# Optimization experiments

Hardware: AMD Instinct MI355X
Metric: run time of the kernel (lower is better)

Reference implementation:

```python
import jax, jax.numpy as jnp
import numpy as np
from jax import lax

K = 8            # number of object slots
H = 250          # hidden / fc_size
EPS = 1e-5
DN = ('NCHW', 'OIHW', 'NCHW')


def ln_all(x):
    # F.layer_norm over all non-batch dims, no affine params (torch init: w=1,b=0)
    ax = tuple(range(1, x.ndim))
    m = jnp.mean(x, ax, keepdims=True)
    v = jnp.var(x, ax, keepdims=True)
    return (x - m) * lax.rsqrt(v + EPS)


def ln_last(x):
    # nn.LayerNorm(feat) -> last dim only
    m = jnp.mean(x, -1, keepdims=True)
    v = jnp.var(x, -1, keepdims=True)
    return (x - m) * lax.rsqrt(v + EPS)


def conv(x, w, b):
    # torch Conv2d(k=4, s=2, p=1), NCHW
    y = lax.conv_general_dilated(x, w, (2, 2), [(1, 1), (1, 1)], dimension_numbers=DN)
    return y + b[None, :, None, None]


def up4(x):
    return jnp.repeat(jnp.repeat(x, 4, axis=2), 4, axis=3)


def setup_inputs():
    ks = jax.random.split(jax.random.key(0), 20)
    bk = 48 * K
    p = lambda i, shape, s: jax.random.normal(ks[i], shape, jnp.float32) * s
    z = lambda n: jnp.zeros((n,), jnp.float32)
    return dict(
        x=p(0, (bk, 4096), 1.0),
        state=p(1, (bk, H), 1.0),
        # encoder convs (OIHW) + fc
        c1w=p(2, (16, 1, 4, 4), 0.25), c1b=z(16),
        c2w=p(3, (32, 16, 4, 4), 0.06), c2b=z(32),
        c3w=p(4, (64, 32, 4, 4), 0.04), c3b=z(64),
        efc_w=p(5, (4096, 512), 0.016), efc_b=z(512),
        # R_NEM (weights stored as [in, out])
        renc_w=p(6, (H, H), 0.06), renc_b=z(H),
        core_w=p(7, (2 * H, H), 0.045), core_b=z(H),
        ctx_w=p(8, (H, H), 0.06), ctx_b=z(H),
        att1_w=p(9, (H, 100), 0.06), att1_b=z(100),
        att2_w=p(10, (100, 1), 0.1), att2_b=z(1),
        out_w=p(11, (2 * H + 512, H), 0.03), out_b=z(H),
        # decoder fcs + convs
        dfc1_w=p(12, (H, 512), 0.06), dfc1_b=z(512),
        dfc2_w=p(13, (512, 4096), 0.045), dfc2_b=z(4096),
        d1w=p(14, (32, 64, 4, 4), 0.03), d1b=z(32),
        d2w=p(15, (16, 32, 4, 4), 0.045), d2b=z(16),
        d3w=p(16, (1, 16, 4, 4), 0.06), d3b=z(1),
    )


def reference(x, state, c1w, c1b, c2w, c2b, c3w, c3b, efc_w, efc_b,
              renc_w, renc_b, core_w, core_b, ctx_w, ctx_b,
              att1_w, att1_b, att2_w, att2_b, out_w, out_b,
              dfc1_w, dfc1_b, dfc2_w, dfc2_b, d1w, d1b, d2w, d2b, d3w, d3b):
    bk = x.shape[0]
    b = bk // K

    # ---------------- EncoderLayer ----------------
    def inwrap(h, w, bias):  # InputWrapper conv branch: NHWC -> permute(0,3,2,1) -> conv -> back
        y = conv(jnp.transpose(h, (0, 3, 2, 1)), w, bias)
        return jax.nn.elu(ln_all(jnp.transpose(y, (0, 3, 2, 1))))

    h = x.reshape(bk, 64, 64, 1)
    h = inwrap(h, c1w, c1b)                 # (bk,32,32,16)
    h = inwrap(h, c2w, c2b)                 # (bk,16,16,32)
    h = inwrap(h, c3w, c3b)                 # (bk,8,8,64)
    h = h.reshape(bk, -1)                   # (bk,4096)
    h = jax.nn.elu(ln_last(h @ efc_w + efc_b))   # (bk,512)

    # ---------------- R_NEM (RecurrentLayer) ----------------
    s1 = jax.nn.relu(ln_last(state @ renc_w + renc_b))   # (bk,H)
    s1r = s1.reshape(b, K, H)
    idx = np.array([[j for j in range(K) if j != i] for i in range(K)])  # (K,K-1)
    cs = s1r[:, idx, :]                                    # context: (b,K,K-1,H)
    fs = jnp.broadcast_to(s1r[:, :, None, :], cs.shape)    # focus copies
    pair = jnp.concatenate([fs, cs], axis=-1)              # (b,K,K-1,2H)
    core = jax.nn.relu(ln_last(pair @ core_w + core_b))    # (b,K,K-1,H)
    ctx = jax.nn.relu(ln_last(core @ ctx_w + ctx_b))       # (b,K,K-1,H)
    att = jax.nn.sigmoid(jnp.tanh(ln_last(core @ att1_w + att1_b)) @ att2_w + att2_b)  # (b,K,K-1,1)
    effect = jnp.sum(ctx * att, axis=2).reshape(bk, H)     # attention-weighted sum over K-1
    total = jnp.concatenate([s1, effect, h], axis=1)       # (bk, 2H+512)
    new_state = total @ out_w + out_b                      # (bk,H)
    xr = jax.nn.sigmoid(ln_last(new_state))
    state_out = jax.nn.sigmoid(new_state)

    # ---------------- DecoderLayer ----------------
    d = jax.nn.relu(ln_last(xr @ dfc1_w + dfc1_b))         # (bk,512)
    d = jax.nn.relu(ln_last(d @ dfc2_w + dfc2_b))          # (bk,4096)
    d = d.reshape(bk, 8, 8, 64)

    def outwrap(t, w, bias):
        y = conv(up4(jnp.transpose(t, (0, 3, 2, 1))), w, bias)
        return jnp.transpose(y, (0, 3, 2, 1))

    d = jax.nn.relu(ln_all(outwrap(d, d1w, d1b)))          # (bk,16,16,32)
    d = jax.nn.relu(ln_all(outwrap(d, d2w, d2b)))          # (bk,32,32,16)
    d = jax.nn.sigmoid(outwrap(d, d3w, d3b))               # (bk,64,64,1), no LN
    x_out = d.reshape(bk, -1)                              # (bk,4096)
    return x_out, state_out
```

## Files before the change

### kernel.cpp

```cpp
#include <hip/hip_runtime.h>
#include <hip/hip_bf16.h>
#include <math.h>

#define ST_ENC2 0
#define ST_ENC3 1
#define ST_DEC1 2
#define ST_DEC2 3
#define ST_ENC1 4

typedef __attribute__((ext_vector_type(8))) short bf16x8;
typedef __attribute__((ext_vector_type(4))) float f32x4;

__device__ __forceinline__ float eluf(float v){ return v > 0.f ? v : expm1f(v); }
__device__ __forceinline__ float sigf(float v){ return 1.f/(1.f+expf(-v)); }
__device__ __forceinline__ unsigned short f2bf(float f){
  unsigned u = __float_as_uint(f);
  u += 0x7FFFu + ((u >> 16) & 1u);
  return (unsigned short)(u >> 16);
}
__device__ __forceinline__ float bf2f(short s){
  return __uint_as_float(((unsigned)(unsigned short)s) << 16);
}

__device__ __forceinline__ void block_reduce2(float& a, float& b, float* sbuf){
  __syncthreads();
  for (int off = 32; off; off >>= 1){
    a += __shfl_down(a, off);
    b += __shfl_down(b, off);
  }
  int lane = threadIdx.x & 63, w = threadIdx.x >> 6;
  if (lane == 0){ sbuf[2*w] = a; sbuf[2*w+1] = b; }
  __syncthreads();
  if (threadIdx.x == 0){
    int nw = blockDim.x >> 6;
    float sa = 0.f, sb = 0.f;
    for (int i = 0; i < nw; i++){ sa += sbuf[2*i]; sb += sbuf[2*i+1]; }
    sbuf[0] = sa; sbuf[1] = sb;
  }
  __syncthreads();
  a = sbuf[0]; b = sbuf[1];
}
// ... 14 lines not shown
}
__device__ __forceinline__ void fold_elem(const float* __restrict__ w, float* __restrict__ CW,
                                          int O, int I, int l){
  int o = l % O; int q = l / O;
  int da = q & 1, db = (q>>1)&1, pa = (q>>2)&1, pb = (q>>3)&1, i = q>>4;
  CW[(((pb*2+pa)*4 + db*2+da)*I + i)*O + o] = fold_sum(w, O, I, o, i, pa, pb, da, db);
}
__device__ __forceinline__ void cvtc2_elem(const float* __restrict__ w, short* __restrict__ D, int l){
  int i = l & 15, t = (l>>4) & 15, o = l>>8;
  D[l] = (short)f2bf(w[(o*16 + i)*16 + t]);
}
__device__ __forceinline__ void cvtc3_elem(const float* __restrict__ w, short* __restrict__ D, int l){
  int i = l & 31, t = (l>>5) & 15, o = l>>9;
  D[l] = (short)f2bf(w[(o*32 + i)*16 + t]);
}
__device__ __forceinline__ void foldd1_elem(const float* __restrict__ w, short* __restrict__ D, int l){
  int i = l & 63, tap = (l>>6)&3, o = (l>>8)&31, ph = l>>13;
  D[l] = (short)f2bf(fold_sum(w, 32, 64, o, i, ph&1, ph>>1, tap&1, tap>>1));
}
__device__ __forceinline__ void foldd2_elem(const float* __restrict__ w, short* __restrict__ D, int l){
  int i = l & 31, tap = (l>>5)&3, o = (l>>7)&15, ph = l>>11;
  D[l] = (short)f2bf(fold_sum(w, 16, 32, o, i, ph&1, ph>>1, tap&1, tap>>1));
}

__global__ __launch_bounds__(256) void prep_combined(
  const float* __restrict__ efc,  short* __restrict__ Defc,
  const float* __restrict__ dfc2, short* __restrict__ Ddfc2,
  const float* __restrict__ outw, short* __restrict__ Dout,
  const float* __restrict__ corew,short* __restrict__ Dcore,
  const float* __restrict__ dfc1, short* __restrict__ Ddfc1,
  const float* __restrict__ renc, short* __restrict__ Drenc,
  const float* __restrict__ ctx,  short* __restrict__ Dctx,
  const float* __restrict__ att1, short* __restrict__ Datt1,
  float* __restrict__ stat,
  const float* __restrict__ d3w, float* __restrict__ CWT3,
  const float* __restrict__ c2w, short* __restrict__ BtC2,
  const float* __restrict__ c3w, short* __restrict__ BtC3,
  const float* __restrict__ d1w, short* __restrict__ BD1,
  const float* __restrict__ d2w, short* __restrict__ BD2,
  const float* __restrict__ state, short* __restrict__ SBF,
  short* __restrict__ TOTb)
{
  int bx = blockIdx.x;
  if (bx >= 1192){
    const int S0=3840, F3=S0+256, P2=F3+8192, P3=P2+32768, P4=P3+32768, P5=P4+8192,
              ST=P5+98304, TOTAL=ST+4608;
    for (int l = (bx-1192)*256 + threadIdx.x; l < TOTAL; l += 256*256){
      if (l < S0)      stat[l] = 0.f;
      else if (l < F3) fold_elem(d3w, CWT3, 1, 16, l - S0);
      else if (l < P2) cvtc2_elem(c2w, BtC2, l - F3);
      else if (l < P3) cvtc3_elem(c3w, BtC3, l - P2);
      else if (l < P4) foldd1_elem(d1w, BD1, l - P3);
      else if (l < P5) foldd2_elem(d2w, BD2, l - P4);
      else if (l < ST){
        int q = l - P5;
        int n = q >> 8, k = q & 255;
        SBF[q] = (k < 250) ? (short)f2bf(state[n*250 + k]) : (short)0;
      } else {
        int q = l - ST;
        int row = q / 12, cc = q % 12;
        int col = cc < 6 ? 250 + cc : 506 + (cc - 6);
        TOTb[row*1024 + col] = 0;
      }
    }
    return;
  }
  const float* W; short* D; int K, N, Kp, base, mode = 0;
  if      (bx < 512) { W=efc;  D=Defc;  K=4096; N=512;  Kp=4096; base=0;    }
  else if (bx < 1024){ W=dfc2; D=Ddfc2; K=512;  N=4096; Kp=512;  base=512;  }
  else if (bx < 1088){ W=outw; D=Dout;  K=1012; N=250;  Kp=1024; base=1024; mode=2; }
  else if (bx < 1120){ W=corew;D=Dcore; K=500;  N=250;  Kp=512;  base=1088; mode=1; }
  else if (bx < 1152){ W=dfc1; D=Ddfc1; K=250;  N=512;  Kp=256;  base=1120; }
  else if (bx < 1168){ W=renc; D=Drenc; K=250;  N=250;  Kp=256;  base=1152; }
  else if (bx < 1184){ W=ctx;  D=Dctx;  K=250;  N=250;  Kp=256;  base=1168; }
  else               { W=att1; D=Datt1; K=250;  N=100;  Kp=256;  base=1184; }
  int t = bx - base;
  int tpr = Kp >> 6;
  int tk = t % tpr, tn = t / tpr;
  __shared__ short tile[64][65];
  int c = threadIdx.x & 63, r4 = threadIdx.x >> 6;
  int n0 = tn*64, k0 = tk*64;
  #pragma unroll 4
  for (int p = 0; p < 16; p++){
    int r = r4*16 + p;
    int k = k0 + r, n = n0 + c;
    int ksrc = k; bool valid;
    if (mode == 0) valid = (k < K);
    else if (mode == 1){ valid = (k < 250) || (k >= 256 && k < 506); ksrc = k < 256 ? k : k - 6; }
    else { valid = (k < 250) || (k >= 256 && k < 506) || (k >= 512);
           ksrc = k < 256 ? k : (k < 512 ? k - 6 : k - 12); }
    float v = (valid && n < N) ? W[(size_t)ksrc*N + n] : 0.f;
    tile[c][r] = (short)f2bf(v);
  }
  __syncthreads();
  #pragma unroll 4
  for (int p = 0; p < 16; p++){
    int nn = r4*16 + p;
    int n = n0 + nn;
    if (n < N) D[(size_t)n*Kp + k0 + c] = tile[nn][c];
  }
}

__global__ __launch_bounds__(256) void cvt_ln_elu(
    const short* __restrict__ inb, const float* __restrict__ stat, short* __restrict__ outb)
{
  int n = blockIdx.x, tid = threadIdx.x;
  float sm = stat[n*2], sq = stat[n*2+1];
  float m = sm*(1.f/4096.f), rs = rsqrtf(sq*(1.f/4096.f) - m*m + 1e-5f);
  const short* ip = inb + (size_t)n*4096;
  short* op = outb + (size_t)n*4096;
  for (int l = tid*4; l < 4096; l += 1024){
    uint2 rv = *(const uint2*)&ip[l];
    float v0 = bf2f((short)(rv.x & 0xFFFF)), v1 = bf2f((short)(rv.x >> 16));
    float v2 = bf2f((short)(rv.y & 0xFFFF)), v3 = bf2f((short)(rv.y >> 16));
    uint2 pk;
    pk.x = f2bf(eluf((v0-m)*rs)) | ((unsigned)f2bf(eluf((v1-m)*rs))<<16);
    pk.y = f2bf(eluf((v2-m)*rs)) | ((unsigned)f2bf(eluf((v3-m)*rs))<<16);
    *(uint2*)&op[l] = pk;
  }
}

__global__ __launch_bounds__(256) void gemm_mfma(
    const short* __restrict__ Ab, const short* __restrict__ Bt,
    float* __restrict__ P, int M, int N, int Kp, int Kc)
{
  __shared__ __align__(16) short As[64*32];
  __shared__ __align__(16) short Bs[64*32];
  int tid = threadIdx.x;
  int bm = blockIdx.y*64, bn = blockIdx.x*64;
  int kb = blockIdx.z * Kc;
  int kend = kb + Kc;

  int r = tid >> 2, c = tid & 3;
  const short* Arow = Ab + (size_t)(bm + r)*Kp;
  int gn = bn + r;
  bool bval = gn < N;
  const short* Brow = Bt + (size_t)gn*Kp;

  uint4 hA, hB;
  auto load_regs = [&](int k0){
    hA = *(const uint4*)&Arow[k0 + c*8];
    hB = bval ? *(const uint4*)&Brow[k0 + c*8] : make_uint4(0,0,0,0);
  };
  auto write_lds = [&](){
    *(uint4*)&As[r*32 + c*8] = hA;
    *(uint4*)&Bs[r*32 + c*8] = hB;
  };

  int wave = tid >> 6;
  int ln = tid & 15, quad = (tid >> 4) & 3;
  int wr = (wave >> 1) * 32, wc = (wave & 1) * 32;

  f32x4 zero = {0.f, 0.f, 0.f, 0.f};
  f32x4 acc[2][2] = {{zero, zero}, {zero, zero}};
// ... 122 lines not shown
    float v = (rowbuf[c]-m)*r;
    if (act == 1) v = fmaxf(v, 0.f);
    else if (act == 2) v = eluf(v);
    else if (act == 3) v = tanhf(v);
    if (obf) ((short*)outp)[(size_t)row*os + c] = f2bf(v);
    else     ((float*)outp)[(size_t)row*os + c] = v;
  }
}

__global__ __launch_bounds__(256) void reduce_ns(
    const float* __restrict__ Pp, const float* __restrict__ bias,
    short* __restrict__ XRb, float* __restrict__ so, int M, int N, int KS)
{
  __shared__ float rowbuf[256];
  __shared__ float sbuf[16];
  int row = blockIdx.x;
  size_t MN = (size_t)M*N;
  float s = 0.f, s2 = 0.f;
  for (int c = threadIdx.x; c < N; c += 256){
    float v = bias[c];
    for (int ks = 0; ks < KS; ks++) v += Pp[ks*MN + (size_t)row*N + c];
    rowbuf[c] = v; s += v; s2 += v*v;
  }
  block_reduce2(s, s2, sbuf);
  float m = s / N;
  float r = rsqrtf(s2/N - m*m + 1e-5f);
  for (int c = threadIdx.x; c < N; c += 256){
    float v = rowbuf[c];
    XRb[(size_t)row*256 + c] = f2bf(sigf((v-m)*r));
    so[(size_t)row*N + c] = sigf(v);
  }
}

__global__ __launch_bounds__(256) void ctx_att_effect(
    const float* __restrict__ Pc, const float* __restrict__ ctx_b,
    const float* __restrict__ Pa, const float* __restrict__ att1_b,
    const float* __restrict__ w2, const float* __restrict__ b2,
    short* __restrict__ tot)
{
  __shared__ float ctxs[7][256];
  __shared__ float att_s[8];
  __shared__ float sbuf[16];
  int fi = blockIdx.x, tid = threadIdx.x;
  const size_t MN = (size_t)2688*250, MN2 = (size_t)2688*100;
  for (int jj = 0; jj < 7; jj++){
    int row = fi*7 + jj;
    float s = 0.f, s2 = 0.f, v = 0.f;
    if (tid < 250){
      v = ctx_b[tid] + Pc[(size_t)row*250 + tid] + Pc[MN + (size_t)row*250 + tid];
      s = v; s2 = v*v;
    }
    block_reduce2(s, s2, sbuf);
    float m = s*(1.f/250.f);
    float r = rsqrtf(s2*(1.f/250.f) - m*m + 1e-5f);
    if (tid < 250) ctxs[jj][tid] = fmaxf((v-m)*r, 0.f);
    float va = 0.f; s = 0.f; s2 = 0.f;
    if (tid < 100){
      va = att1_b[tid];
      #pragma unroll
      for (int ks = 0; ks < 4; ks++) va += Pa[ks*MN2 + (size_t)row*100 + tid];
      s = va; s2 = va*va;
    }
    block_reduce2(s, s2, sbuf);
    m = s*0.01f;
    r = rsqrtf(s2*0.01f - m*m + 1e-5f);
    float d = (tid < 100) ? tanhf((va-m)*r)*w2[tid] : 0.f;
    float dummy = 0.f;
    block_reduce2(d, dummy, sbuf);
    if (tid == 0) att_s[jj] = sigf(d + b2[0]);
  }
  __syncthreads();
  if (tid < 250){
    float s = 0.f;
    #pragma unroll
    for (int q = 0; q < 7; q++) s += ctxs[q][tid]*att_s[q];
    tot[(size_t)fi*1024 + 256 + tid] = f2bf(s);
  }
}

__global__ __launch_bounds__(256) void enc_conv1_ig(
    const float* __restrict__ x, const float* __restrict__ w, const float* __restrict__ bias,
    short* __restrict__ outp, float* __restrict__ stat)
{
  __shared__ __align__(16) float in_t[66*68];
  __shared__ float sbuf[16];
  int n = blockIdx.x, tid = threadIdx.x;
  for (int l = tid; l < 66*68; l += 256) in_t[l] = 0.f;
  __syncthreads();
  const float* xin = x + (size_t)n*4096;
  for (int l4 = tid; l4 < 1024; l4 += 256){
    float4 v = *(const float4*)&xin[l4*4];
    int aa = (l4*4) >> 6, bb = (l4*4) & 63;
    float* dst = &in_t[(aa+1)*68 + bb + 1];
    dst[0]=v.x; dst[1]=v.y; dst[2]=v.z; dst[3]=v.w;
  }
  int o = tid & 15;
  float wr[16];
  #pragma unroll
  for (int t = 0; t < 16; t++) wr[t] = w[o*16 + t];
  float bv = bias[o];
  __syncthreads();
  float s = 0.f, s2 = 0.f;
  short* op = outp + (size_t)n*16384;
  for (int r = 0; r < 64; r++){
    int idx = tid + (r<<8);
    int bq = (idx>>4)&31, aq = idx>>9;
    int a0 = 2*aq, b0 = 2*bq;
    float acc = bv;
    #pragma unroll
    for (int kw = 0; kw < 4; kw++){
      const float* row = &in_t[(a0+kw)*68 + b0];
      float2 p0 = *(const float2*)&row[0];
      float2 p1 = *(const float2*)&row[2];
      acc += p0.x*wr[0*4+kw] + p0.y*wr[1*4+kw] + p1.x*wr[2*4+kw] + p1.y*wr[3*4+kw];
    }
    op[idx] = f2bf(acc);
    s += acc; s2 += acc*acc;
  }
  block_reduce2(s, s2, sbuf);
  if (tid == 0){ atomicAdd(&stat[n*2], s); atomicAdd(&stat[n*2+1], s2); }
}

__global__ __launch_bounds__(256) void enc_conv2_mfma(
    const short* __restrict__ in, const short* __restrict__ Bt, const float* __restrict__ bias,
    const float* __restrict__ stat_in, short* __restrict__ outp, float* __restrict__ stat)
{
  __shared__ __align__(16) short in_t[34*34*16];
  __shared__ float sbuf[16];
  int n = blockIdx.x, tid = threadIdx.x;
  float smv = stat_in[n*2], sqv = stat_in[n*2+1];
  float m = smv*(1.f/16384.f), rs = rsqrtf(sqv*(1.f/16384.f) - m*m + 1e-5f);
  for (int l = tid; l < 34*34*16/4; l += 256) ((unsigned long long*)in_t)[l] = 0ull;
  __syncthreads();
  const short* ip = in + (size_t)n*16384;
  for (int l = tid; l < 4096; l += 256){
    int i4 = l & 3, bb = (l>>2) & 31, aa = l>>7;
    uint2 rv = *(const uint2*)&ip[aa*512 + bb*16 + i4*4];
    float v0 = bf2f((short)(rv.x & 0xFFFF)), v1 = bf2f((short)(rv.x >> 16));
    float v2 = bf2f((short)(rv.y & 0xFFFF)), v3 = bf2f((short)(rv.y >> 16));
    uint2 pk;
    pk.x = f2bf(eluf((v0-m)*rs)) | ((unsigned)f2bf(eluf((v1-m)*rs))<<16);
    pk.y = f2bf(eluf((v2-m)*rs)) | ((unsigned)f2bf(eluf((v3-m)*rs))<<16);
    *(uint2*)&in_t[((aa+1)*34 + (bb+1))*16 + i4*4] = pk;
  }
  int wave = tid>>6, ln = tid&15, quad = (tid>>4)&3;
  bf16x8 bfr[2][8];
  #pragma unroll
  for (int nt = 0; nt < 2; nt++){
    const short* Brow = Bt + (nt*16 + ln)*256;
    #pragma unroll
    for (int ks = 0; ks < 8; ks++)
      bfr[nt][ks] = *(const bf16x8*)&Brow[ks*32 + quad*8];
  }
  __syncthreads();
  f32x4 z = {0.f,0.f,0.f,0.f};
  f32x4 acc[2][4] = {{z,z,z,z},{z,z,z,z}};
  int tapq = quad>>1, io = (quad&1)*8;
  #pragma unroll
  for (int ks = 0; ks < 8; ks++){
    int t = 2*ks + tapq;
    int kh = t>>2, kw = t&3;
    #pragma unroll
    for (int mt = 0; mt < 4; mt++){
      int p = (wave*4 + mt)*16 + ln;
      int oa = p>>4, ob = p&15;
      bf16x8 a = *(const bf16x8*)&in_t[((2*oa+kw)*34 + (2*ob+kh))*16 + io];
      acc[0][mt] = __builtin_amdgcn_mfma_f32_16x16x32_bf16(a, bfr[0][ks], acc[0][mt],0,0,0);
      acc[1][mt] = __builtin_amdgcn_mfma_f32_16x16x32_bf16(a, bfr[1][ks], acc[1][mt],0,0,0);
    }
  }
  float s = 0.f, s2 = 0.f;
  short* op = outp + (size_t)n*8192;
  #pragma unroll
  for (int nt = 0; nt < 2; nt++){
    int o = nt*16 + ln;
    float bz = bias[o];
    #pragma unroll
    for (int mt = 0; mt < 4; mt++)
      #pragma unroll
      for (int j = 0; j < 4; j++){
        int p = (wave*4 + mt)*16 + quad*4 + j;
        float v = acc[nt][mt][j] + bz;
        s += v; s2 += v*v;
        int oa = p>>4, ob = p&15;
        op[oa*512 + ob*32 + o] = f2bf(v);
      }
  }
  block_reduce2(s, s2, sbuf);
  if (tid == 0){ atomicAdd(&stat[n*2], s); atomicAdd(&stat[n*2+1], s2); }
}

__global__ __launch_bounds__(256) void enc_conv3_mfma(
    const short* __restrict__ in, const short* __restrict__ Bt, const float* __restrict__ bias,
    const float* __restrict__ stat_in, short* __restrict__ outp, float* __restrict__ stat)
{
  __shared__ __align__(16) short in_t[18*18*32];
  __shared__ float sbuf[16];
  int n = blockIdx.x, tid = threadIdx.x;
  float smv = stat_in[n*2], sqv = stat_in[n*2+1];
  float m = smv*(1.f/8192.f), rs = rsqrtf(sqv*(1.f/8192.f) - m*m + 1e-5f);
  for (int l = tid; l < 18*18*32/4; l += 256) ((unsigned long long*)in_t)[l] = 0ull;
  __syncthreads();
  const short* ip = in + (size_t)n*8192;
  for (int l = tid; l < 2048; l += 256){
    int i4 = l & 7, bb = (l>>3)&15, aa = l>>7;
    uint2 rv = *(const uint2*)&ip[aa*512 + bb*32 + i4*4];
    float v0 = bf2f((short)(rv.x & 0xFFFF)), v1 = bf2f((short)(rv.x >> 16));
    float v2 = bf2f((short)(rv.y & 0xFFFF)), v3 = bf2f((short)(rv.y >> 16));
    uint2 pk;
    pk.x = f2bf(eluf((v0-m)*rs)) | ((unsigned)f2bf(eluf((v1-m)*rs))<<16);
    pk.y = f2bf(eluf((v2-m)*rs)) | ((unsigned)f2bf(eluf((v3-m)*rs))<<16);
    *(uint2*)&in_t[((aa+1)*18 + (bb+1))*32 + i4*4] = pk;
  }
  int wave = tid>>6, ln = tid&15, quad = (tid>>4)&3;
  int o = wave*16 + ln;
  bf16x8 bfr[16];
  {
    const short* Brow = Bt + o*512;
    #pragma unroll
    for (int ks = 0; ks < 16; ks++)
      bfr[ks] = *(const bf16x8*)&Brow[ks*32 + quad*8];
  }
  __syncthreads();
  f32x4 z = {0.f,0.f,0.f,0.f};
  f32x4 acc[4] = {z,z,z,z};
  #pragma unroll
  for (int ks = 0; ks < 16; ks++){
    int kh = ks>>2, kw = ks&3;
    #pragma unroll
    for (int mt = 0; mt < 4; mt++){
      int p = mt*16 + ln;
      int oa = p>>3, ob = p&7;
      bf16x8 a = *(const bf16x8*)&in_t[((2*oa+kw)*18 + (2*ob+kh))*32 + quad*8];
      acc[mt] = __builtin_amdgcn_mfma_f32_16x16x32_bf16(a, bfr[ks], acc[mt],0,0,0);
    }
  }
  float s = 0.f, s2 = 0.f;
  float bz = bias[o];
  short* op = outp + (size_t)n*4096;
  #pragma unroll
  for (int mt = 0; mt < 4; mt++)
    #pragma unroll
    for (int j = 0; j < 4; j++){
      int p = mt*16 + quad*4 + j;
      int oa = p>>3, ob = p&7;
      float v = acc[mt][j] + bz;
      s += v; s2 += v*v;
      op[oa*512 + ob*64 + o] = f2bf(v);
    }
  block_reduce2(s, s2, sbuf);
  if (tid == 0){ atomicAdd(&stat[n*2], s); atomicAdd(&stat[n*2+1], s2); }
}

__global__ __launch_bounds__(256) void dec_conv1_mfma(
    const short* __restrict__ in, const short* __restrict__ Bd, const float* __restrict__ bias,
    short* __restrict__ outp, float* __restrict__ stat)
{
  __shared__ __align__(16) short in_t[10*10*64];
  __shared__ float sbuf[16];
  int n = blockIdx.x, tid = threadIdx.x;
  for (int l = tid; l < 10*10*64/4; l += 256) ((unsigned long long*)in_t)[l] = 0ull;
  __syncthreads();
  const short* ip = in + (size_t)n*4096;
  for (int l = tid; l < 1024; l += 256){
    int i4 = l & 15, sb = (l>>4)&7, sa = l>>7;
    *(uint2*)&in_t[((sa+1)*10 + (sb+1))*64 + i4*4] = *(const uint2*)&ip[sa*512 + sb*64 + i4*4];
  }
  int wave = tid>>6, ln = tid&15, quad = (tid>>4)&3;
  int pa = wave & 1, pb = wave >> 1;
  bf16x8 bfr[2][8];
  #pragma unroll
  for (int nt = 0; nt < 2; nt++){
    const short* Brow = Bd + (wave*32 + nt*16 + ln)*256;
    #pragma unroll
    for (int ks = 0; ks < 8; ks++)
      bfr[nt][ks] = *(const bf16x8*)&Brow[ks*32 + quad*8];
  }
  __syncthreads();
  f32x4 z = {0.f,0.f,0.f,0.f};
  f32x4 acc[2][4] = {{z,z,z,z},{z,z,z,z}};
  #pragma unroll
  for (int ks = 0; ks < 8; ks++){
    int tap = ks>>1, ibase = (ks&1)*32 + quad*8;
    int da = tap & 1, db = tap >> 1;
    #pragma unroll
    for (int mt = 0; mt < 4; mt++){
      int p = mt*16 + ln;
      int ta = p>>3, tb = p&7;
      bf16x8 a = *(const bf16x8*)&in_t[((ta+da+pa)*10 + (tb+db+pb))*64 + ibase];
      acc[0][mt] = __builtin_amdgcn_mfma_f32_16x16x32_bf16(a, bfr[0][ks], acc[0][mt],0,0,0);
      acc[1][mt] = __builtin_amdgcn_mfma_f32_16x16x32_bf16(a, bfr[1][ks], acc[1][mt],0,0,0);
    }
  }
  float s = 0.f, s2 = 0.f;
  short* op = outp + (size_t)n*8192;
  #pragma unroll
  for (int nt = 0; nt < 2; nt++){
    int o = nt*16 + ln;
    float bz = bias[o];
    #pragma unroll
    for (int mt = 0; mt < 4; mt++)
      #pragma unroll
      for (int j = 0; j < 4; j++){
        int p = mt*16 + quad*4 + j;
        int ta = p>>3, tb = p&7;
        float v = acc[nt][mt][j] + bz;
        s += v; s2 += v*v;
        op[(2*ta+pa)*512 + (2*tb+pb)*32 + o] = f2bf(v);
      }
  }
  block_reduce2(s, s2, sbuf);
  if (tid == 0){ atomicAdd(&stat[n*2], s); atomicAdd(&stat[n*2+1], s2); }
}

__global__ __launch_bounds__(256) void dec_conv2_mfma(
    const short* __restrict__ in, const short* __restrict__ Bd, const float* __restrict__ bias,
    const float* __restrict__ stat_in, short* __restrict__ outp, float* __restrict__ stat)
{
  __shared__ __align__(16) short in_t[18*18*32];
  __shared__ float sbuf[16];
  int n = blockIdx.x, tid = threadIdx.x;
  float smv = stat_in[n*2], sqv = stat_in[n*2+1];
  float m = smv*(1.f/8192.f), rs = rsqrtf(sqv*(1.f/8192.f) - m*m + 1e-5f);
  for (int l = tid; l < 18*18*32/4; l += 256) ((unsigned long long*)in_t)[l] = 0ull;
  __syncthreads();
  const short* ip = in + (size_t)n*8192;
  for (int l = tid; l < 2048; l += 256){
    int i4 = l & 7, sb = (l>>3)&15, sa = l>>7;
    uint2 rv = *(const uint2*)&ip[sa*512 + sb*32 + i4*4];
    float v0 = bf2f((short)(rv.x & 0xFFFF)), v1 = bf2f((short)(rv.x >> 16));
    float v2 = bf2f((short)(rv.y & 0xFFFF)), v3 = bf2f((short)(rv.y >> 16));
    uint2 pk;
    pk.x = f2bf(fmaxf((v0-m)*rs,0.f)) | ((unsigned)f2bf(fmaxf((v1-m)*rs,0.f))<<16);
    pk.y = f2bf(fmaxf((v2-m)*rs,0.f)) | ((unsigned)f2bf(fmaxf((v3-m)*rs,0.f))<<16);
    *(uint2*)&in_t[((sa+1)*18 + (sb+1))*32 + i4*4] = pk;
  }
  int wave = tid>>6, ln = tid&15, quad = (tid>>4)&3;
  int pa = wave & 1, pb = wave >> 1;
  bf16x8 bfr[4];
  {
    const short* Brow = Bd + (wave*16 + ln)*128;
    #pragma unroll
    for (int ks = 0; ks < 4; ks++)
      bfr[ks] = *(const bf16x8*)&Brow[ks*32 + quad*8];
  }
  __syncthreads();
  f32x4 z = {0.f,0.f,0.f,0.f};
  f32x4 acc[16] = {z,z,z,z,z,z,z,z,z,z,z,z,z,z,z,z};
  #pragma unroll
  for (int ks = 0; ks < 4; ks++){
    int da = ks & 1, db = ks >> 1;
    #pragma unroll
    for (int mt = 0; mt < 16; mt++){
      int p = mt*16 + ln;
      int ta = p>>4, tb = p&15;
      bf16x8 a = *(const bf16x8*)&in_t[((ta+da+pa)*18 + (tb+db+pb))*32 + quad*8];
      acc[mt] = __builtin_amdgcn_mfma_f32_16x16x32_bf16(a, bfr[ks], acc[mt],0,0,0);
    }
  }
  float s = 0.f, s2 = 0.f;
  float bz = bias[ln];
  short* op = outp + (size_t)n*16384;
  #pragma unroll
  for (int mt = 0; mt < 16; mt++)
    #pragma unroll
    for (int j = 0; j < 4; j++){
      int p = mt*16 + quad*4 + j;
      int ta = p>>4, tb = p&15;
      float v = acc[mt][j] + bz;
      s += v; s2 += v*v;
      op[(2*ta+pa)*512 + (2*tb+pb)*16 + ln] = f2bf(v);
    }
  block_reduce2(s, s2, sbuf);
  if (tid == 0){ atomicAdd(&stat[n*2], s); atomicAdd(&stat[n*2+1], s2); }
}

__global__ __launch_bounds__(256) void dec_conv3_ig(
    const short* __restrict__ in, const float* __restrict__ CWT, const float* __restrict__ bias,
    const float* __restrict__ stat_in, float* __restrict__ outp)
{
  __shared__ __align__(16) float in_t[9792];
  __shared__ __align__(16) float wl[256];
  int bx = blockIdx.x;
  int n = bx >> 1, b0 = (bx & 1) * 32, tb0 = b0 >> 1;
  int tid = threadIdx.x;
  float sm = stat_in[n*2], sq = stat_in[n*2+1];
  float m = sm*(1.f/16384.f), rs = rsqrtf(sq*(1.f/16384.f) - m*m + 1e-5f);
  const short* ip = in + (size_t)n*16384;
  for (int l = tid; l < 9792; l += 256){
    int i = l & 15, sb = (l >> 4) % 18, sap = l / 288;
    int sa = sap - 1, sbg = tb0 - 1 + sb;
    float v = 0.f;
    if ((unsigned)sa < 32u && (unsigned)sbg < 32u)
      v = fmaxf((bf2f(ip[sa*512 + sbg*16 + i])-m)*rs, 0.f);
    in_t[(sap*18 + sb)*16 + i] = v;
  }
  for (int l = tid; l < 256; l += 256) wl[l] = CWT[l];
  __syncthreads();
  float bv = bias[0];
  int bl = tid & 31, ath = tid >> 5;
  int b = b0 + bl;
  int tb = b >> 1, pb = b & 1;
  float* op = outp + (size_t)n*4096;
  #pragma unroll
  for (int j = 0; j < 8; j++){
    int a = ath*8 + j;
    int ta = a >> 1, pa = a & 1;
    float4 s4 = make_float4(0.f,0.f,0.f,0.f);
    #pragma unroll
    for (int db = 0; db < 2; db++){
      int sb = tb + db + (pb ? 0 : -1);
      int sbl = sb - (tb0 - 1);
      #pragma unroll
      for (int da = 0; da < 2; da++){
        int sa = ta + da + (pa ? 0 : -1);
        int sap = sa + 1;
        const float4* A4 = (const float4*)&in_t[(sap*18 + sbl)*16];
        const float4* B4 = (const float4*)&wl[((pb*2+pa)*4 + db*2+da)*16];
        #pragma unroll
        for (int q = 0; q < 4; q++){
          float4 av = A4[q], bw = B4[q];
          s4.x += av.x*bw.x; s4.y += av.y*bw.y;
          s4.z += av.z*bw.z; s4.w += av.w*bw.w;
        }
      }
    }
    op[a*64 + b] = sigf(bv + s4.x + s4.y + s4.z + s4.w);
// ... 11 lines not shown
  const float* c2b    = (const float*)d_in[5];
  const float* c3w    = (const float*)d_in[6];
  const float* c3b    = (const float*)d_in[7];
  const float* efc_w  = (const float*)d_in[8];
  const float* efc_b  = (const float*)d_in[9];
  const float* renc_w = (const float*)d_in[10];
  const float* renc_b = (const float*)d_in[11];
  const float* core_w = (const float*)d_in[12];
  const float* core_b = (const float*)d_in[13];
  const float* ctx_w  = (const float*)d_in[14];
  const float* ctx_b  = (const float*)d_in[15];
  const float* att1_w = (const float*)d_in[16];
  const float* att1_b = (const float*)d_in[17];
  const float* att2_w = (const float*)d_in[18];
  const float* att2_b = (const float*)d_in[19];
  const float* out_w  = (const float*)d_in[20];
  const float* out_b  = (const float*)d_in[21];
  const float* dfc1_w = (const float*)d_in[22];
  const float* dfc1_b = (const float*)d_in[23];
  const float* dfc2_w = (const float*)d_in[24];
  const float* dfc2_b = (const float*)d_in[25];
  const float* d1w    = (const float*)d_in[26];
  const float* d1b    = (const float*)d_in[27];
  const float* d2w    = (const float*)d_in[28];
  const float* d2b    = (const float*)d_in[29];
  const float* d3w    = (const float*)d_in[30];
  const float* d3b    = (const float*)d_in[31];

  float* wsf = (float*)d_ws;
  size_t o = 0;
  float* PB   = wsf + o; o += (size_t)1600*1024;
  float* PB2  = wsf + o; o += (size_t)2688*100*4;
  float* CWT3 = wsf + o; o += 256;
  float* STAT = wsf + o; o += 5*384*2;
  short* E1b  = (short*)(wsf + o); o += (size_t)384*16384/2;
  short* E2b  = (short*)(wsf + o); o += (size_t)384*8192/2;
  short* E3b  = (short*)(wsf + o); o += (size_t)384*4096/2;
  short* TOTb = (short*)(wsf + o); o += (size_t)384*1024/2;
  short* C1b  = (short*)(wsf + o); o += (size_t)2688*256/2;
  short* XRb  = (short*)(wsf + o); o += (size_t)384*256/2;
  short* G1b  = (short*)(wsf + o); o += (size_t)384*512/2;
  short* ECV  = (short*)(wsf + o); o += (size_t)384*4096/2;
  short* SBF  = (short*)(wsf + o); o += (size_t)384*256/2;
  short* BtC2 = (short*)(wsf + o); o += 8192/2;
  short* BtC3 = (short*)(wsf + o); o += 32768/2;
  short* BD1  = (short*)(wsf + o); o += 32768/2;
  short* BD2  = (short*)(wsf + o); o += 8192/2;
  short* BT_efc  = (short*)(wsf + o); o += 2097152/2;
  short* BT_renc = (short*)(wsf + o); o += 64000/2;
  short* BT_core = (short*)(wsf + o); o += 128000/2;
  short* BT_ctx  = (short*)(wsf + o); o += 64000/2;
  short* BT_att1 = (short*)(wsf + o); o += 25600/2;
  short* BT_out  = (short*)(wsf + o); o += 256000/2;
  short* BT_dfc1 = (short*)(wsf + o); o += 131072/2;
  short* BT_dfc2 = (short*)(wsf + o); o += 2097152/2;
  short* D1b = E2b;
  short* D2b = E1b;
  short* G2b = E3b;

  float* xout = (float*)d_out;
  float* sout = xout + (size_t)384*4096;

  prep_combined<<<1448, 256, 0, stream>>>(
      efc_w, BT_efc, dfc2_w, BT_dfc2, out_w, BT_out, core_w, BT_core,
      dfc1_w, BT_dfc1, renc_w, BT_renc, ctx_w, BT_ctx, att1_w, BT_att1,
      STAT, d3w, CWT3, c2w, BtC2, c3w, BtC3, d1w, BD1, d2w, BD2, state, SBF, TOTb);

  enc_conv1_ig<<<384, 256, 0, stream>>>(x, c1w, c1b, E1b, STAT + ST_ENC1*768);
  enc_conv2_mfma<<<384, 256, 0, stream>>>(E1b, BtC2, c2b, STAT + ST_ENC1*768, E2b, STAT + ST_ENC2*768);
  enc_conv3_mfma<<<384, 256, 0, stream>>>(E2b, BtC3, c3b, STAT + ST_ENC2*768, E3b, STAT + ST_ENC3*768);
  cvt_ln_elu<<<384, 256, 0, stream>>>(E3b, STAT + ST_ENC3*768, ECV);
  gemm_mfma<<<dim3(8,6,8), 256, 0, stream>>>(ECV, BT_efc, PB, 384, 512, 4096, 512);
  reduce_ln<<<384, 256, 0, stream>>>(PB, efc_b, TOTb+512, 384, 512, 8, 1024, 2, 1);

  gemm_mfma<<<dim3(4,6,8), 256, 0, stream>>>(SBF, BT_renc, PB, 384, 250, 256, 32);
  reduce_ln<<<384, 256, 0, stream>>>(PB, renc_b, TOTb, 384, 250, 8, 1024, 1, 1);
  gemm_core_mfma<<<dim3(4,42,2), 256, 0, stream>>>(TOTb, BT_core, PB, 2688, 250, 256);
  reduce_ln<<<2688, 256, 0, stream>>>(PB, core_b, C1b, 2688, 250, 2, 256, 1, 1);
  gemm_mfma<<<dim3(4,42,2), 256, 0, stream>>>(C1b, BT_ctx, PB, 2688, 250, 256, 128);
  gemm_mfma<<<dim3(2,42,4), 256, 0, stream>>>(C1b, BT_att1, PB2, 2688, 100, 256, 64);
  ctx_att_effect<<<384, 256, 0, stream>>>(PB, ctx_b, PB2, att1_b, att2_w, att2_b, TOTb);

  gemm_mfma<<<dim3(4,6,8), 256, 0, stream>>>(TOTb, BT_out, PB, 384, 250, 1024, 128);
  reduce_ns<<<384, 256, 0, stream>>>(PB, out_b, XRb, sout, 384, 250, 8);

  gemm_mfma<<<dim3(8,6,4), 256, 0, stream>>>(XRb, BT_dfc1, PB, 384, 512, 256, 64);
  reduce_ln<<<384, 256, 0, stream>>>(PB, dfc1_b, G1b, 384, 512, 4, 512, 1, 1);
  gemm_mfma<<<dim3(64,6,1), 256, 0, stream>>>(G1b, BT_dfc2, PB, 384, 4096, 512, 512);
  reduce_ln<<<384, 256, 0, stream>>>(PB, dfc2_b, G2b, 384, 4096, 1, 4096, 1, 1);

  dec_conv1_mfma<<<384, 256, 0, stream>>>(G2b, BD1, d1b, D1b, STAT + ST_DEC1*768);
  dec_conv2_mfma<<<384, 256, 0, stream>>>(D1b, BD2, d2b, STAT + ST_DEC1*768, D2b, STAT + ST_DEC2*768);
  dec_conv3_ig<<<768, 256, 0, stream>>>(D2b, CWT3, d3b, STAT + ST_DEC2*768, xout);

  (void)in_sizes; (void)n_in; (void)out_size; (void)ws_size;
}
```

Baseline: 356.4 us.

## Apply per-sample LayerNorm in conv producers, drop stat atomics and cvt kernel

Each conv kernel already holds the whole per-sample output, so it now computes the LayerNorm statistics itself, normalizes, and writes the activated values. Consumers just copy them into LDS. This removes the global atomic stat buffer, its zeroing in the prep kernel, and the separate cvt_ln_elu launch. The attention kernel is also reworked to one wave per row with shuffle reductions instead of a serial loop of block reductions. In exchange, enc_conv1 gains a 32KB LDS staging buffer, which may lower occupancy.

```diff
diff --git a/kernel.cpp b/kernel.cpp
--- a/kernel.cpp
+++ b/kernel.cpp
@@ -1,12 +1,6 @@
 #include <hip/hip_runtime.h>
 #include <hip/hip_bf16.h>
 #include <math.h>
-
-#define ST_ENC2 0
-#define ST_ENC3 1
-#define ST_DEC1 2
-#define ST_DEC2 3
-#define ST_ENC1 4
 
 typedef __attribute__((ext_vector_type(8))) short bf16x8;
 typedef __attribute__((ext_vector_type(4))) float f32x4;
@@ -87,7 +81,6 @@
   const float* __restrict__ renc, short* __restrict__ Drenc,
   const float* __restrict__ ctx,  short* __restrict__ Dctx,
   const float* __restrict__ att1, short* __restrict__ Datt1,
-  float* __restrict__ stat,
   const float* __restrict__ d3w, float* __restrict__ CWT3,
   const float* __restrict__ c2w, short* __restrict__ BtC2,
   const float* __restrict__ c3w, short* __restrict__ BtC3,
@@ -98,11 +91,10 @@
 {
   int bx = blockIdx.x;
   if (bx >= 1192){
-    const int S0=3840, F3=S0+256, P2=F3+8192, P3=P2+32768, P4=P3+32768, P5=P4+8192,
+    const int F3=256, P2=F3+8192, P3=P2+32768, P4=P3+32768, P5=P4+8192,
               ST=P5+98304, TOTAL=ST+4608;
     for (int l = (bx-1192)*256 + threadIdx.x; l < TOTAL; l += 256*256){
-      if (l < S0)      stat[l] = 0.f;
-      else if (l < F3) fold_elem(d3w, CWT3, 1, 16, l - S0);
+      if (l < F3)      fold_elem(d3w, CWT3, 1, 16, l);
       else if (l < P2) cvtc2_elem(c2w, BtC2, l - F3);
       else if (l < P3) cvtc3_elem(c3w, BtC3, l - P2);
       else if (l < P4) foldd1_elem(d1w, BD1, l - P3);
@@ -156,25 +148,6 @@
   }
 }
 
-__global__ __launch_bounds__(256) void cvt_ln_elu(
-    const short* __restrict__ inb, const float* __restrict__ stat, short* __restrict__ outb)
-{
-  int n = blockIdx.x, tid = threadIdx.x;
-  float sm = stat[n*2], sq = stat[n*2+1];
-  float m = sm*(1.f/4096.f), rs = rsqrtf(sq*(1.f/4096.f) - m*m + 1e-5f);
-  const short* ip = inb + (size_t)n*4096;
-  short* op = outb + (size_t)n*4096;
-  for (int l = tid*4; l < 4096; l += 1024){
-    uint2 rv = *(const uint2*)&ip[l];
-    float v0 = bf2f((short)(rv.x & 0xFFFF)), v1 = bf2f((short)(rv.x >> 16));
-    float v2 = bf2f((short)(rv.y & 0xFFFF)), v3 = bf2f((short)(rv.y >> 16));
-    uint2 pk;
-    pk.x = f2bf(eluf((v0-m)*rs)) | ((unsigned)f2bf(eluf((v1-m)*rs))<<16);
-    pk.y = f2bf(eluf((v2-m)*rs)) | ((unsigned)f2bf(eluf((v3-m)*rs))<<16);
-    *(uint2*)&op[l] = pk;
-  }
-}
-
 __global__ __launch_bounds__(256) void gemm_mfma(
     const short* __restrict__ Ab, const short* __restrict__ Bt,
     float* __restrict__ P, int M, int N, int Kp, int Kc)
@@ -363,57 +336,79 @@
   }
 }
 
-__global__ __launch_bounds__(256) void ctx_att_effect(
+__global__ __launch_bounds__(448) void ctx_att_effect(
     const float* __restrict__ Pc, const float* __restrict__ ctx_b,
     const float* __restrict__ Pa, const float* __restrict__ att1_b,
     const float* __restrict__ w2, const float* __restrict__ b2,
     short* __restrict__ tot)
 {
-  __shared__ float ctxs[7][256];
-  __shared__ float att_s[8];
-  __shared__ float sbuf[16];
+  __shared__ float ctxs[7][250];
+  __shared__ float att_s[7];
   int fi = blockIdx.x, tid = threadIdx.x;
+  int jj = tid >> 6, lane = tid & 63;
   const size_t MN = (size_t)2688*250, MN2 = (size_t)2688*100;
-  for (int jj = 0; jj < 7; jj++){
-    int row = fi*7 + jj;
-    float s = 0.f, s2 = 0.f, v = 0.f;
-    if (tid < 250){
-      v = ctx_b[tid] + Pc[(size_t)row*250 + tid] + Pc[MN + (size_t)row*250 + tid];
-      s = v; s2 = v*v;
-    }
-    block_reduce2(s, s2, sbuf);
-    float m = s*(1.f/250.f);
-    float r = rsqrtf(s2*(1.f/250.f) - m*m + 1e-5f);
-    if (tid < 250) ctxs[jj][tid] = fmaxf((v-m)*r, 0.f);
-    float va = 0.f; s = 0.f; s2 = 0.f;
-    if (tid < 100){
-      va = att1_b[tid];
+  int row = fi*7 + jj;
+  float vv[4];
+  float s = 0.f, s2 = 0.f;
+  #pragma unroll
+  for (int t = 0; t < 4; t++){
+    int c = lane + t*64;
+    float v = 0.f;
+    if (c < 250) v = ctx_b[c] + Pc[(size_t)row*250 + c] + Pc[MN + (size_t)row*250 + c];
+    vv[t] = v; s += v; s2 += v*v;
+  }
+  #pragma unroll
+  for (int off = 32; off; off >>= 1){ s += __shfl_down(s, off); s2 += __shfl_down(s2, off); }
+  s = __shfl(s, 0); s2 = __shfl(s2, 0);
+  float m = s*(1.f/250.f);
+  float r = rsqrtf(s2*(1.f/250.f) - m*m + 1e-5f);
+  #pragma unroll
+  for (int t = 0; t < 4; t++){
+    int c = lane + t*64;
+    if (c < 250) ctxs[jj][c] = fmaxf((vv[t]-m)*r, 0.f);
+  }
+  float va[2];
+  s = 0.f; s2 = 0.f;
+  #pragma unroll
+  for (int t = 0; t < 2; t++){
+    int c = lane + t*64;
+    float v = 0.f;
+    if (c < 100){
+      v = att1_b[c];
       #pragma unroll
-      for (int ks = 0; ks < 4; ks++) va += Pa[ks*MN2 + (size_t)row*100 + tid];
-      s = va; s2 = va*va;
-    }
-    block_reduce2(s, s2, sbuf);
-    m = s*0.01f;
-    r = rsqrtf(s2*0.01f - m*m + 1e-5f);
-    float d = (tid < 100) ? tanhf((va-m)*r)*w2[tid] : 0.f;
-    float dummy = 0.f;
-    block_reduce2(d, dummy, sbuf);
-    if (tid == 0) att_s[jj] = sigf(d + b2[0]);
-  }
-  __syncthreads();
-  if (tid < 250){
-    float s = 0.f;
-    #pragma unroll
-    for (int q = 0; q < 7; q++) s += ctxs[q][tid]*att_s[q];
-    tot[(size_t)fi*1024 + 256 + tid] = f2bf(s);
+      for (int ks = 0; ks < 4; ks++) v += Pa[ks*MN2 + (size_t)row*100 + c];
+    }
+    va[t] = v; s += v; s2 += v*v;
+  }
+  #pragma unroll
+  for (int off = 32; off; off >>= 1){ s += __shfl_down(s, off); s2 += __shfl_down(s2, off); }
+  s = __shfl(s, 0); s2 = __shfl(s2, 0);
+  m = s*0.01f;
+  r = rsqrtf(s2*0.01f - m*m + 1e-5f);
+  float d = 0.f;
+  #pragma unroll
+  for (int t = 0; t < 2; t++){
+    int c = lane + t*64;
+    if (c < 100) d += tanhf((va[t]-m)*r)*w2[c];
+  }
+  #pragma unroll
+  for (int off = 32; off; off >>= 1) d += __shfl_down(d, off);
+  if (lane == 0) att_s[jj] = sigf(d + b2[0]);
+  __syncthreads();
+  for (int h = tid; h < 250; h += 448){
+    float sum = 0.f;
+    #pragma unroll
+    for (int q = 0; q < 7; q++) sum += ctxs[q][h]*att_s[q];
+    tot[(size_t)fi*1024 + 256 + h] = f2bf(sum);
   }
 }
 
 __global__ __launch_bounds__(256) void enc_conv1_ig(
     const float* __restrict__ x, const float* __restrict__ w, const float* __restrict__ bias,
-    short* __restrict__ outp, float* __restrict__ stat)
+    short* __restrict__ outp)
 {
   __shared__ __align__(16) float in_t[66*68];
+  __shared__ short rawb[16384];
   __shared__ float sbuf[16];
   int n = blockIdx.x, tid = threadIdx.x;
   for (int l = tid; l < 66*68; l += 256) in_t[l] = 0.f;
@@ -432,7 +427,6 @@
   float bv = bias[o];
   __syncthreads();
   float s = 0.f, s2 = 0.f;
-  short* op = outp + (size_t)n*16384;
   for (int r = 0; r < 64; r++){
     int idx = tid + (r<<8);
     int bq = (idx>>4)&31, aq = idx>>9;
@@ -445,34 +439,32 @@
       float2 p1 = *(const float2*)&row[2];
       acc += p0.x*wr[0*4+kw] + p0.y*wr[1*4+kw] + p1.x*wr[2*4+kw] + p1.y*wr[3*4+kw];
     }
-    op[idx] = f2bf(acc);
+    rawb[idx] = f2bf(acc);
     s += acc; s2 += acc*acc;
   }
   block_reduce2(s, s2, sbuf);
-  if (tid == 0){ atomicAdd(&stat[n*2], s); atomicAdd(&stat[n*2+1], s2); }
+  float m = s*(1.f/16384.f);
+  float rs = rsqrtf(s2*(1.f/16384.f) - m*m + 1e-5f);
+  short* op = outp + (size_t)n*16384;
+  for (int l = tid; l < 16384; l += 256){
+    float v = bf2f(rawb[l]);
+    op[l] = f2bf(eluf((v-m)*rs));
+  }
 }
 
 __global__ __launch_bounds__(256) void enc_conv2_mfma(
     const short* __restrict__ in, const short* __restrict__ Bt, const float* __restrict__ bias,
-    const float* __restrict__ stat_in, short* __restrict__ outp, float* __restrict__ stat)
+    short* __restrict__ outp)
 {
   __shared__ __align__(16) short in_t[34*34*16];
   __shared__ float sbuf[16];
   int n = blockIdx.x, tid = threadIdx.x;
-  float smv = stat_in[n*2], sqv = stat_in[n*2+1];
-  float m = smv*(1.f/16384.f), rs = rsqrtf(sqv*(1.f/16384.f) - m*m + 1e-5f);
   for (int l = tid; l < 34*34*16/4; l += 256) ((unsigned long long*)in_t)[l] = 0ull;
   __syncthreads();
   const short* ip = in + (size_t)n*16384;
   for (int l = tid; l < 4096; l += 256){
     int i4 = l & 3, bb = (l>>2) & 31, aa = l>>7;
-    uint2 rv = *(const uint2*)&ip[aa*512 + bb*16 + i4*4];
-    float v0 = bf2f((short)(rv.x & 0xFFFF)), v1 = bf2f((short)(rv.x >> 16));
-    float v2 = bf2f((short)(rv.y & 0xFFFF)), v3 = bf2f((short)(rv.y >> 16));
-    uint2 pk;
-    pk.x = f2bf(eluf((v0-m)*rs)) | ((unsigned)f2bf(eluf((v1-m)*rs))<<16);
-    pk.y = f2bf(eluf((v2-m)*rs)) | ((unsigned)f2bf(eluf((v3-m)*rs))<<16);
-    *(uint2*)&in_t[((aa+1)*34 + (bb+1))*16 + i4*4] = pk;
+    *(uint2*)&in_t[((aa+1)*34 + (bb+1))*16 + i4*4] = *(const uint2*)&ip[aa*512 + bb*16 + i4*4];
   }
   int wave = tid>>6, ln = tid&15, quad = (tid>>4)&3;
   bf16x8 bfr[2][8];
@@ -501,47 +493,48 @@
     }
   }
   float s = 0.f, s2 = 0.f;
+  #pragma unroll
+  for (int nt = 0; nt < 2; nt++){
+    float bz = bias[nt*16 + ln];
+    #pragma unroll
+    for (int mt = 0; mt < 4; mt++)
+      #pragma unroll
+      for (int j = 0; j < 4; j++){
+        float v = acc[nt][mt][j] + bz;
+        acc[nt][mt][j] = v; s += v; s2 += v*v;
+      }
+  }
+  block_reduce2(s, s2, sbuf);
+  float m = s*(1.f/8192.f);
+  float rs = rsqrtf(s2*(1.f/8192.f) - m*m + 1e-5f);
   short* op = outp + (size_t)n*8192;
   #pragma unroll
   for (int nt = 0; nt < 2; nt++){
     int o = nt*16 + ln;
-    float bz = bias[o];
     #pragma unroll
     for (int mt = 0; mt < 4; mt++)
       #pragma unroll
       for (int j = 0; j < 4; j++){
         int p = (wave*4 + mt)*16 + quad*4 + j;
-        float v = acc[nt][mt][j] + bz;
-        s += v; s2 += v*v;
         int oa = p>>4, ob = p&15;
-        op[oa*512 + ob*32 + o] = f2bf(v);
+        op[oa*512 + ob*32 + o] = f2bf(eluf((acc[nt][mt][j]-m)*rs));
       }
   }
-  block_reduce2(s, s2, sbuf);
-  if (tid == 0){ atomicAdd(&stat[n*2], s); atomicAdd(&stat[n*2+1], s2); }
 }
 
 __global__ __launch_bounds__(256) void enc_conv3_mfma(
     const short* __restrict__ in, const short* __restrict__ Bt, const float* __restrict__ bias,
-    const float* __restrict__ stat_in, short* __restrict__ outp, float* __restrict__ stat)
+    short* __restrict__ outp)
 {
   __shared__ __align__(16) short in_t[18*18*32];
   __shared__ float sbuf[16];
   int n = blockIdx.x, tid = threadIdx.x;
-  float smv = stat_in[n*2], sqv = stat_in[n*2+1];
-  float m = smv*(1.f/8192.f), rs = rsqrtf(sqv*(1.f/8192.f) - m*m + 1e-5f);
   for (int l = tid; l < 18*18*32/4; l += 256) ((unsigned long long*)in_t)[l] = 0ull;
   __syncthreads();
   const short* ip = in + (size_t)n*8192;
   for (int l = tid; l < 2048; l += 256){
     int i4 = l & 7, bb = (l>>3)&15, aa = l>>7;
-    uint2 rv = *(const uint2*)&ip[aa*512 + bb*32 + i4*4];
-    float v0 = bf2f((short)(rv.x & 0xFFFF)), v1 = bf2f((short)(rv.x >> 16));
-    float v2 = bf2f((short)(rv.y & 0xFFFF)), v3 = bf2f((short)(rv.y >> 16));
-    uint2 pk;
-    pk.x = f2bf(eluf((v0-m)*rs)) | ((unsigned)f2bf(eluf((v1-m)*rs))<<16);
-    pk.y = f2bf(eluf((v2-m)*rs)) | ((unsigned)f2bf(eluf((v3-m)*rs))<<16);
-    *(uint2*)&in_t[((aa+1)*18 + (bb+1))*32 + i4*4] = pk;
+    *(uint2*)&in_t[((aa+1)*18 + (bb+1))*32 + i4*4] = *(const uint2*)&ip[aa*512 + bb*32 + i4*4];
   }
   int wave = tid>>6, ln = tid&15, quad = (tid>>4)&3;
   int o = wave*16 + ln;
@@ -568,6 +561,16 @@
   }
   float s = 0.f, s2 = 0.f;
   float bz = bias[o];
+  #pragma unroll
+  for (int mt = 0; mt < 4; mt++)
+    #pragma unroll
+    for (int j = 0; j < 4; j++){
+      float v = acc[mt][j] + bz;
+      acc[mt][j] = v; s += v; s2 += v*v;
+    }
+  block_reduce2(s, s2, sbuf);
+  float m = s*(1.f/4096.f);
+  float rs = rsqrtf(s2*(1.f/4096.f) - m*m + 1e-5f);
   short* op = outp + (size_t)n*4096;
   #pragma unroll
   for (int mt = 0; mt < 4; mt++)
@@ -575,17 +578,13 @@
     for (int j = 0; j < 4; j++){
       int p = mt*16 + quad*4 + j;
       int oa = p>>3, ob = p&7;
-      float v = acc[mt][j] + bz;
-      s += v; s2 += v*v;
-      op[oa*512 + ob*64 + o] = f2bf(v);
-    }
-  block_reduce2(s, s2, sbuf);
-  if (tid == 0){ atomicAdd(&stat[n*2], s); atomicAdd(&stat[n*2+1], s2); }
+      op[oa*512 + ob*64 + o] = f2bf(eluf((acc[mt][j]-m)*rs));
+    }
 }
 
 __global__ __launch_bounds__(256) void dec_conv1_mfma(
     const short* __restrict__ in, const short* __restrict__ Bd, const float* __restrict__ bias,
-    short* __restrict__ outp, float* __restrict__ stat)
+    short* __restrict__ outp)
 {
   __shared__ __align__(16) short in_t[10*10*64];
   __shared__ float sbuf[16];
@@ -624,47 +623,48 @@
     }
   }
   float s = 0.f, s2 = 0.f;
+  #pragma unroll
+  for (int nt = 0; nt < 2; nt++){
+    float bz = bias[nt*16 + ln];
+    #pragma unroll
+    for (int mt = 0; mt < 4; mt++)
+      #pragma unroll
+      for (int j = 0; j < 4; j++){
+        float v = acc[nt][mt][j] + bz;
+        acc[nt][mt][j] = v; s += v; s2 += v*v;
+      }
+  }
+  block_reduce2(s, s2, sbuf);
+  float m = s*(1.f/8192.f);
+  float rs = rsqrtf(s2*(1.f/8192.f) - m*m + 1e-5f);
   short* op = outp + (size_t)n*8192;
   #pragma unroll
   for (int nt = 0; nt < 2; nt++){
     int o = nt*16 + ln;
-    float bz = bias[o];
     #pragma unroll
     for (int mt = 0; mt < 4; mt++)
       #pragma unroll
       for (int j = 0; j < 4; j++){
         int p = mt*16 + quad*4 + j;
         int ta = p>>3, tb = p&7;
-        float v = acc[nt][mt][j] + bz;
-        s += v; s2 += v*v;
-        op[(2*ta+pa)*512 + (2*tb+pb)*32 + o] = f2bf(v);
+        op[(2*ta+pa)*512 + (2*tb+pb)*32 + o] = f2bf(fmaxf((acc[nt][mt][j]-m)*rs, 0.f));
       }
   }
-  block_reduce2(s, s2, sbuf);
-  if (tid == 0){ atomicAdd(&stat[n*2], s); atomicAdd(&stat[n*2+1], s2); }
 }
 
 __global__ __launch_bounds__(256) void dec_conv2_mfma(
     const short* __restrict__ in, const short* __restrict__ Bd, const float* __restrict__ bias,
-    const float* __restrict__ stat_in, short* __restrict__ outp, float* __restrict__ stat)
+    short* __restrict__ outp)
 {
   __shared__ __align__(16) short in_t[18*18*32];
   __shared__ float sbuf[16];
   int n = blockIdx.x, tid = threadIdx.x;
-  float smv = stat_in[n*2], sqv = stat_in[n*2+1];
-  float m = smv*(1.f/8192.f), rs = rsqrtf(sqv*(1.f/8192.f) - m*m + 1e-5f);
   for (int l = tid; l < 18*18*32/4; l += 256) ((unsigned long long*)in_t)[l] = 0ull;
   __syncthreads();
   const short* ip = in + (size_t)n*8192;
   for (int l = tid; l < 2048; l += 256){
     int i4 = l & 7, sb = (l>>3)&15, sa = l>>7;
-    uint2 rv = *(const uint2*)&ip[sa*512 + sb*32 + i4*4];
-    float v0 = bf2f((short)(rv.x & 0xFFFF)), v1 = bf2f((short)(rv.x >> 16));
-    float v2 = bf2f((short)(rv.y & 0xFFFF)), v3 = bf2f((short)(rv.y >> 16));
-    uint2 pk;
-    pk.x = f2bf(fmaxf((v0-m)*rs,0.f)) | ((unsigned)f2bf(fmaxf((v1-m)*rs,0.f))<<16);
-    pk.y = f2bf(fmaxf((v2-m)*rs,0.f)) | ((unsigned)f2bf(fmaxf((v3-m)*rs,0.f))<<16);
-    *(uint2*)&in_t[((sa+1)*18 + (sb+1))*32 + i4*4] = pk;
+    *(uint2*)&in_t[((sa+1)*18 + (sb+1))*32 + i4*4] = *(const uint2*)&ip[sa*512 + sb*32 + i4*4];
   }
   int wave = tid>>6, ln = tid&15, quad = (tid>>4)&3;
   int pa = wave & 1, pb = wave >> 1;
@@ -691,6 +691,16 @@
   }
   float s = 0.f, s2 = 0.f;
   float bz = bias[ln];
+  #pragma unroll
+  for (int mt = 0; mt < 16; mt++)
+    #pragma unroll
+    for (int j = 0; j < 4; j++){
+      float v = acc[mt][j] + bz;
+      acc[mt][j] = v; s += v; s2 += v*v;
+    }
+  block_reduce2(s, s2, sbuf);
+  float m = s*(1.f/16384.f);
+  float rs = rsqrtf(s2*(1.f/16384.f) - m*m + 1e-5f);
   short* op = outp + (size_t)n*16384;
   #pragma unroll
   for (int mt = 0; mt < 16; mt++)
@@ -698,32 +708,26 @@
     for (int j = 0; j < 4; j++){
       int p = mt*16 + quad*4 + j;
       int ta = p>>4, tb = p&15;
-      float v = acc[mt][j] + bz;
-      s += v; s2 += v*v;
-      op[(2*ta+pa)*512 + (2*tb+pb)*16 + ln] = f2bf(v);
-    }
-  block_reduce2(s, s2, sbuf);
-  if (tid == 0){ atomicAdd(&stat[n*2], s); atomicAdd(&stat[n*2+1], s2); }
+      op[(2*ta+pa)*512 + (2*tb+pb)*16 + ln] = f2bf(fmaxf((acc[mt][j]-m)*rs, 0.f));
+    }
 }
 
 __global__ __launch_bounds__(256) void dec_conv3_ig(
     const short* __restrict__ in, const float* __restrict__ CWT, const float* __restrict__ bias,
-    const float* __restrict__ stat_in, float* __restrict__ outp)
+    float* __restrict__ outp)
 {
   __shared__ __align__(16) float in_t[9792];
   __shared__ __align__(16) float wl[256];
   int bx = blockIdx.x;
   int n = bx >> 1, b0 = (bx & 1) * 32, tb0 = b0 >> 1;
   int tid = threadIdx.x;
-  float sm = stat_in[n*2], sq = stat_in[n*2+1];
-  float m = sm*(1.f/16384.f), rs = rsqrtf(sq*(1.f/16384.f) - m*m + 1e-5f);
   const short* ip = in + (size_t)n*16384;
   for (int l = tid; l < 9792; l += 256){
     int i = l & 15, sb = (l >> 4) % 18, sap = l / 288;
     int sa = sap - 1, sbg = tb0 - 1 + sb;
     float v = 0.f;
     if ((unsigned)sa < 32u && (unsigned)sbg < 32u)
-      v = fmaxf((bf2f(ip[sa*512 + sbg*16 + i])-m)*rs, 0.f);
+      v = bf2f(ip[sa*512 + sbg*16 + i]);
     in_t[(sap*18 + sb)*16 + i] = v;
   }
   for (int l = tid; l < 256; l += 256) wl[l] = CWT[l];
@@ -801,7 +805,6 @@
   float* PB   = wsf + o; o += (size_t)1600*1024;
   float* PB2  = wsf + o; o += (size_t)2688*100*4;
   float* CWT3 = wsf + o; o += 256;
-  float* STAT = wsf + o; o += 5*384*2;
   short* E1b  = (short*)(wsf + o); o += (size_t)384*16384/2;
   short* E2b  = (short*)(wsf + o); o += (size_t)384*8192/2;
   short* E3b  = (short*)(wsf + o); o += (size_t)384*4096/2;
@@ -809,7 +812,6 @@
   short* C1b  = (short*)(wsf + o); o += (size_t)2688*256/2;
   short* XRb  = (short*)(wsf + o); o += (size_t)384*256/2;
   short* G1b  = (short*)(wsf + o); o += (size_t)384*512/2;
-  short* ECV  = (short*)(wsf + o); o += (size_t)384*4096/2;
   short* SBF  = (short*)(wsf + o); o += (size_t)384*256/2;
   short* BtC2 = (short*)(wsf + o); o += 8192/2;
   short* BtC3 = (short*)(wsf + o); o += 32768/2;
@@ -833,13 +835,12 @@
   prep_combined<<<1448, 256, 0, stream>>>(
       efc_w, BT_efc, dfc2_w, BT_dfc2, out_w, BT_out, core_w, BT_core,
       dfc1_w, BT_dfc1, renc_w, BT_renc, ctx_w, BT_ctx, att1_w, BT_att1,
-      STAT, d3w, CWT3, c2w, BtC2, c3w, BtC3, d1w, BD1, d2w, BD2, state, SBF, TOTb);
-
-  enc_conv1_ig<<<384, 256, 0, stream>>>(x, c1w, c1b, E1b, STAT + ST_ENC1*768);
-  enc_conv2_mfma<<<384, 256, 0, stream>>>(E1b, BtC2, c2b, STAT + ST_ENC1*768, E2b, STAT + ST_ENC2*768);
-  enc_conv3_mfma<<<384, 256, 0, stream>>>(E2b, BtC3, c3b, STAT + ST_ENC2*768, E3b, STAT + ST_ENC3*768);
-  cvt_ln_elu<<<384, 256, 0, stream>>>(E3b, STAT + ST_ENC3*768, ECV);
-  gemm_mfma<<<dim3(8,6,8), 256, 0, stream>>>(ECV, BT_efc, PB, 384, 512, 4096, 512);
+      d3w, CWT3, c2w, BtC2, c3w, BtC3, d1w, BD1, d2w, BD2, state, SBF, TOTb);
+
+  enc_conv1_ig<<<384, 256, 0, stream>>>(x, c1w, c1b, E1b);
+  enc_conv2_mfma<<<384, 256, 0, stream>>>(E1b, BtC2, c2b, E2b);
+  enc_conv3_mfma<<<384, 256, 0, stream>>>(E2b, BtC3, c3b, E3b);
+  gemm_mfma<<<dim3(8,6,8), 256, 0, stream>>>(E3b, BT_efc, PB, 384, 512, 4096, 512);
   reduce_ln<<<384, 256, 0, stream>>>(PB, efc_b, TOTb+512, 384, 512, 8, 1024, 2, 1);
 
   gemm_mfma<<<dim3(4,6,8), 256, 0, stream>>>(SBF, BT_renc, PB, 384, 250, 256, 32);
@@ -848,7 +849,7 @@
   reduce_ln<<<2688, 256, 0, stream>>>(PB, core_b, C1b, 2688, 250, 2, 256, 1, 1);
   gemm_mfma<<<dim3(4,42,2), 256, 0, stream>>>(C1b, BT_ctx, PB, 2688, 250, 256, 128);
   gemm_mfma<<<dim3(2,42,4), 256, 0, stream>>>(C1b, BT_att1, PB2, 2688, 100, 256, 64);
-  ctx_att_effect<<<384, 256, 0, stream>>>(PB, ctx_b, PB2, att1_b, att2_w, att2_b, TOTb);
+  ctx_att_effect<<<384, 448, 0, stream>>>(PB, ctx_b, PB2, att1_b, att2_w, att2_b, TOTb);
 
   gemm_mfma<<<dim3(4,6,8), 256, 0, stream>>>(TOTb, BT_out, PB, 384, 250, 1024, 128);
   reduce_ns<<<384, 256, 0, stream>>>(PB, out_b, XRb, sout, 384, 250, 8);
@@ -858,9 +859,9 @@
   gemm_mfma<<<dim3(64,6,1), 256, 0, stream>>>(G1b, BT_dfc2, PB, 384, 4096, 512, 512);
   reduce_ln<<<384, 256, 0, stream>>>(PB, dfc2_b, G2b, 384, 4096, 1, 4096, 1, 1);
 
-  dec_conv1_mfma<<<384, 256, 0, stream>>>(G2b, BD1, d1b, D1b, STAT + ST_DEC1*768);
-  dec_conv2_mfma<<<384, 256, 0, stream>>>(D1b, BD2, d2b, STAT + ST_DEC1*768, D2b, STAT + ST_DEC2*768);
-  dec_conv3_ig<<<768, 256, 0, stream>>>(D2b, CWT3, d3b, STAT + ST_DEC2*768, xout);
+  dec_conv1_mfma<<<384, 256, 0, stream>>>(G2b, BD1, d1b, D1b);
+  dec_conv2_mfma<<<384, 256, 0, stream>>>(D1b, BD2, d2b, D2b);
+  dec_conv3_ig<<<768, 256, 0, stream>>>(D2b, CWT3, d3b, xout);
 
   (void)in_sizes; (void)n_in; (void)out_size; (void)ws_size;
 }
```

After: 334.7 us (median of 2 runs). 1.06x faster.
